# Kernel tuning notes

Measured on AMD Instinct MI355X. Metric: run time of the kernel, lower is better.

The kernel has to match this reference:

```python
import jax, jax.numpy as jnp
import numpy as np

B, N, E, DIN, DOUT = 8, 4096, 1024, 256, 256
EPS = 1e-8

def setup_inputs() -> dict:
    key = jax.random.key(0)
    k1, k2, k3, k4 = jax.random.split(key, 4)
    x = jax.random.normal(k1, (B, N, DIN), dtype=jnp.float32)
    H = jax.random.uniform(k2, (B, N, E), dtype=jnp.float32)
    weight = jax.random.normal(k3, (DIN, DOUT), dtype=jnp.float32) * (1.0 / np.sqrt(DOUT))
    bias = jax.random.normal(k4, (DOUT,), dtype=jnp.float32) * (1.0 / np.sqrt(DOUT))
    return {"x": x, "hypergraph_matrix": H, "weight": weight, "bias": bias}

def reference(x, hypergraph_matrix, weight, bias):
    H = hypergraph_matrix                      # [B, N, E]
    d_v = jnp.clip(jnp.sum(H, axis=2), EPS)    # node degrees [B, N]
    d_v_inv_sqrt = d_v ** -0.5
    d_e = jnp.clip(jnp.sum(H, axis=1), EPS)    # hyperedge degrees [B, E]
    d_e_inv = 1.0 / d_e
    # D_v^{-1/2} H D_e^{-1}
    step2 = d_v_inv_sqrt[:, :, None] * H * d_e_inv[:, None, :]   # [B, N, E]
    # (D_v^{-1/2} H D_e^{-1} H^T) D_v^{-1/2}  -- original materializes [B, N, N]
    step3 = jnp.einsum('bne,bme->bnm', step2, H)                 # [B, N, N]
    normalized_matrix = step3 * d_v_inv_sqrt[:, None, :]         # [B, N, N]
    support = jnp.einsum('bnd,df->bnf', x, weight)               # X Theta
    out = jnp.einsum('bnm,bmf->bnf', normalized_matrix, support) + bias
    # dropout is identity in eval / deterministic baseline
    return out
```

## Files before the change

kernel.cpp:

```cpp
#include <hip/hip_runtime.h>
#include <hip/hip_bf16.h>

#define BATCH 8
#define NN 4096
#define EE 1024
#define DIN 256
#define DOUT 256
#define EPS 1e-8f

typedef short bf16x8 __attribute__((ext_vector_type(8)));
typedef float f32x4 __attribute__((ext_vector_type(4)));

__device__ __forceinline__ unsigned short f2bf(float f) {
    unsigned u = __float_as_uint(f);
    return (unsigned short)((u + 0x7FFFu + ((u >> 16) & 1u)) >> 16);
}

__device__ __forceinline__ unsigned pk2(float lo, float hi) {
    __hip_bfloat162 h = __float22bfloat162_rn(float2{lo, hi});
    return *(unsigned*)&h;
}
__device__ __forceinline__ bf16x8 pack8(float4 a, float4 b) {
    union { bf16x8 v; unsigned u[4]; } r;
    r.u[0] = pk2(a.x, a.y); r.u[1] = pk2(a.z, a.w);
    r.u[2] = pk2(b.x, b.y); r.u[3] = pk2(b.z, b.w);
    return r.v;
}

__device__ __forceinline__ void g2l16(const void* g, void* l) {
    __builtin_amdgcn_global_load_lds(
        (const __attribute__((address_space(1))) unsigned*)g,
        (__attribute__((address_space(3))) unsigned*)l, 16, 0, 0);
}


template <int LD>
__device__ __forceinline__ void stage_tile(const unsigned short* src, int k0, short* lds, int tid) {
#pragma unroll
    for (int j = 0; j < 2; ++j) {
        int q = tid + j * 256;
        int r = q >> 2;
        int c = (q ^ (r >> 1)) & 3;
        g2l16(src + (size_t)r * LD + k0 + c * 8, (char*)lds + q * 16);
    }
}

__device__ __forceinline__ bf16x8 frag_ld(const short* lds, int r, int c) {
    int off = (r << 6) | (((c ^ (r >> 1)) & 3) << 4);
    return *(const bf16x8*)((const char*)lds + off);
}

template <int LDA, int LDB>
__device__ __forceinline__ void gemm_core(const unsigned short* A, const unsigned short* B,
                                          int kIters, int k0, f32x4 acc[4][4],
                                          short* As, short* Bs) {
    int tid = threadIdx.x, lane = tid & 63, wave = tid >> 6;
    int wm = (wave >> 1) * 64, wn = (wave & 1) * 64;
    int fr = lane & 15, fc = lane >> 4;
    for (int kt = 0; kt < kIters; ++kt) {
        int k = k0 + kt * 32;
        __syncthreads();
        stage_tile<LDA>(A, k, As, tid);
        stage_tile<LDB>(B, k, Bs, tid);
        __syncthreads();
        bf16x8 av[4], bv[4];
#pragma unroll
        for (int i = 0; i < 4; ++i) av[i] = frag_ld(As, wm + i * 16 + fr, fc);
#pragma unroll
        for (int j = 0; j < 4; ++j) bv[j] = frag_ld(Bs, wn + j * 16 + fr, fc);
#pragma unroll
        for (int i = 0; i < 4; ++i)
#pragma unroll
            for (int j = 0; j < 4; ++j)
                acc[i][j] = __builtin_amdgcn_mfma_f32_16x16x32_bf16(av[i], bv[j], acc[i][j], 0, 0, 0);
    }
}


__global__ __launch_bounds__(256) void prep_tr(const float* __restrict__ H,
                                               unsigned short* __restrict__ Ht,
                                               float* __restrict__ dv_acc,
                                               float* __restrict__ de_acc) {
    __shared__ float tile[64][65];
    int ns = blockIdx.x, et = blockIdx.y, b = blockIdx.z;
    int e0 = et * 64;
    int t = threadIdx.x;
    int r = t >> 2, cq = (t & 3) * 16;
    int c = t >> 2, q = (t & 3) * 16;
    float de_part = 0.f;
    for (int it = 0; it < 8; ++it) {
        int n0 = ns * 512 + it * 64;
        const float* src = H + ((size_t)(b * NN + n0 + r)) * EE + e0 + cq;
        float4 v0 = *(const float4*)(src + 0);
        float4 v1 = *(const float4*)(src + 4);
        float4 v2 = *(const float4*)(src + 8);
        float4 v3 = *(const float4*)(src + 12);
        float rs = v0.x + v0.y + v0.z + v0.w + v1.x + v1.y + v1.z + v1.w +
                   v2.x + v2.y + v2.z + v2.w + v3.x + v3.y + v3.z + v3.w;
        rs += __shfl_down(rs, 2);
        rs += __shfl_down(rs, 1);
        __syncthreads();
        tile[cq + 0][r] = v0.x;  tile[cq + 1][r] = v0.y;  tile[cq + 2][r] = v0.z;  tile[cq + 3][r] = v0.w;
        tile[cq + 4][r] = v1.x;  tile[cq + 5][r] = v1.y;  tile[cq + 6][r] = v1.z;  tile[cq + 7][r] = v1.w;
        tile[cq + 8][r] = v2.x;  tile[cq + 9][r] = v2.y;  tile[cq + 10][r] = v2.z; tile[cq + 11][r] = v2.w;
        tile[cq + 12][r] = v3.x; tile[cq + 13][r] = v3.y; tile[cq + 14][r] = v3.z; tile[cq + 15][r] = v3.w;
        if ((t & 3) == 0) atomicAdd(dv_acc + b * NN + n0 + r, rs);
        __syncthreads();
        float w[16];
#pragma unroll
        for (int j = 0; j < 16; ++j) { w[j] = tile[c][q + j]; de_part += w[j]; }
        bf16x8 p0 = pack8(float4{w[0], w[1], w[2], w[3]}, float4{w[4], w[5], w[6], w[7]});
        bf16x8 p1 = pack8(float4{w[8], w[9], w[10], w[11]}, float4{w[12], w[13], w[14], w[15]});
        unsigned short* dst = Ht + ((size_t)(b * EE + e0 + c)) * NN + n0 + q;
        *(bf16x8*)dst = p0; *(bf16x8*)(dst + 8) = p1;
    }
    de_part += __shfl_down(de_part, 2);
    de_part += __shfl_down(de_part, 1);
    if ((t & 3) == 0) atomicAdd(de_acc + b * EE + e0 + c, de_part);
}

__global__ __launch_bounds__(256) void prep_xw(const float* __restrict__ X,
                                               const float* __restrict__ W,
                                               unsigned short* __restrict__ Xb,
                                               unsigned short* __restrict__ Wt) {
    __shared__ float tile[64][65];
    int bid = blockIdx.x;
    int t = threadIdx.x;
    if (bid < 2048) {
        size_t base = ((size_t)bid * 256 + t) * 16;
        float4 a0 = *(const float4*)(X + base + 0);
        float4 a1 = *(const float4*)(X + base + 4);
        float4 a2 = *(const float4*)(X + base + 8);
        float4 a3 = *(const float4*)(X + base + 12);
        *(bf16x8*)(Xb + base) = pack8(a0, a1);
        *(bf16x8*)(Xb + base + 8) = pack8(a2, a3);
    } else {
        int w = bid - 2048;
        int k0 = (w >> 2) * 64, f0 = (w & 3) * 64;
        int r = t >> 2, cq = (t & 3) * 16;
#pragma unroll
        for (int j = 0; j < 16; j += 4) {
            float4 x4 = *(const float4*)(W + (size_t)(k0 + r) * DOUT + f0 + cq + j);
            tile[r][cq + j] = x4.x; tile[r][cq + j + 1] = x4.y;
            tile[r][cq + j + 2] = x4.z; tile[r][cq + j + 3] = x4.w;
        }
        __syncthreads();
        int c = t >> 2, rq = (t & 3) * 16;
        bf16x8 q0, q1;
#pragma unroll
        for (int j = 0; j < 16; ++j) {
            float x = tile[rq + j][c];
            if (j < 8) q0[j] = (short)f2bf(x); else q1[j - 8] = (short)f2bf(x);
        }
        unsigned short* dst = Wt + (size_t)(f0 + c) * DIN + k0 + rq;
        *(bf16x8*)dst = q0; *(bf16x8*)(dst + 8) = q1;
    }
}


__global__ __launch_bounds__(256) void mfma_xw(const unsigned short* __restrict__ Xb,
                                               const unsigned short* __restrict__ Wt,
                                               const float* __restrict__ dv_acc,
                                               unsigned short* __restrict__ Tt) {
    __shared__ short As[128 * 32], Bs[128 * 32];
    int m0 = blockIdx.x * 128, f0 = blockIdx.y * 128;
    f32x4 acc[4][4] = {};
    gemm_core<DIN, DIN>(Xb + (size_t)m0 * DIN, Wt + (size_t)f0 * DIN, DIN / 32, 0, acc, As, Bs);
    int lane = threadIdx.x & 63, wave = threadIdx.x >> 6;
    int wm = (wave >> 1) * 64, wn = (wave & 1) * 64;
    int rg = (lane >> 4) * 4, cl = lane & 15;
    int b = m0 >> 12, nb = m0 & (NN - 1);
#pragma unroll
    for (int i = 0; i < 4; ++i) {
        int rbase = wm + i * 16 + rg;
        float4 dv = *(const float4*)(dv_acc + m0 + rbase);
        float s0 = rsqrtf(fmaxf(dv.x, EPS)), s1 = rsqrtf(fmaxf(dv.y, EPS));
        float s2 = rsqrtf(fmaxf(dv.z, EPS)), s3 = rsqrtf(fmaxf(dv.w, EPS));
#pragma unroll
        for (int j = 0; j < 4; ++j) {
            int f = f0 + wn + j * 16 + cl;
            f32x4 a = acc[i][j];
            ushort4 o = { f2bf(a.x * s0), f2bf(a.y * s1), f2bf(a.z * s2), f2bf(a.w * s3) };
            *(ushort4*)(Tt + (((size_t)b * DOUT + f) << 12) + nb + rbase) = o;
        }
    }
}

__global__ __launch_bounds__(256) void mfma_ht(const unsigned short* __restrict__ Ht,
                                               const unsigned short* __restrict__ Tt,
                                               float* __restrict__ P) {
    __shared__ short As[128 * 32], Bs[128 * 32];
    int e0 = blockIdx.x * 128, f0 = blockIdx.y * 128;
    int b = blockIdx.z >> 2, s = blockIdx.z & 3;
    f32x4 acc[4][4] = {};
    gemm_core<NN, NN>(Ht + ((size_t)b * EE + e0) * NN, Tt + ((size_t)b * DOUT + f0) * NN,
                      1024 / 32, s * 1024, acc, As, Bs);
    int lane = threadIdx.x & 63, wave = threadIdx.x >> 6;
    int wm = (wave >> 1) * 64, wn = (wave & 1) * 64;
    int rg = (lane >> 4) * 4, cl = lane & 15;
    float* Pb = P + (size_t)s * (BATCH * DOUT * EE) + (size_t)b * (DOUT * EE);
#pragma unroll
    for (int i = 0; i < 4; ++i) {
        int e = e0 + wm + i * 16 + rg;
#pragma unroll
        for (int j = 0; j < 4; ++j) {
            int f = f0 + wn + j * 16 + cl;
            *(f32x4*)(Pb + (size_t)f * EE + e) = acc[i][j];
        }
    }
}

__global__ __launch_bounds__(256) void combine_u(const float* __restrict__ P,
                                                 const float* __restrict__ de_acc,
                                                 unsigned short* __restrict__ Ut) {
    const int PS = BATCH * DOUT * EE;
    int idx = (blockIdx.x * 256 + threadIdx.x) * 4;
    f32x4 s = *(const f32x4*)(P + idx);
    s += *(const f32x4*)(P + PS + idx);
    s += *(const f32x4*)(P + 2 * PS + idx);
    s += *(const f32x4*)(P + 3 * PS + idx);
    int b = idx >> 18, e = idx & (EE - 1);
    float4 de = *(const float4*)(de_acc + b * EE + e);
    ushort4 o = { f2bf(s.x / fmaxf(de.x, EPS)), f2bf(s.y / fmaxf(de.y, EPS)),
                  f2bf(s.z / fmaxf(de.z, EPS)), f2bf(s.w / fmaxf(de.w, EPS)) };
    *(ushort4*)(Ut + idx) = o;
}

__global__ __launch_bounds__(256) void mfma_hu(const unsigned short* __restrict__ Ut,
                                               const float* __restrict__ Hf,
                                               const float* __restrict__ dv_acc,
                                               const float* __restrict__ bias,
                                               float* __restrict__ out) {
    __shared__ short As[128 * 32], Bs[128 * 32];
    int f0 = blockIdx.x * 128, n0 = blockIdx.y * 128, b = blockIdx.z;
    const unsigned short* A = Ut + ((size_t)b * DOUT + f0) * EE;
    const float* Bsrc = Hf + ((size_t)(b * NN + n0)) * EE;
    int tid = threadIdx.x, lane = tid & 63, wave = tid >> 6;
    int wm = (wave >> 1) * 64, wn = (wave & 1) * 64;
    int fr = lane & 15, fc = lane >> 4;
    int br = tid >> 1, bh = tid & 1;
    f32x4 acc[4][4] = {};
    for (int kt = 0; kt < EE / 32; ++kt) {
        int k = kt * 32;
        __syncthreads();
        stage_tile<EE>(A, k, As, tid);
        const float* s = Bsrc + (size_t)br * EE + k + bh * 16;
        float4 x0 = *(const float4*)(s + 0);
        float4 x1 = *(const float4*)(s + 4);
        float4 x2 = *(const float4*)(s + 8);
        float4 x3 = *(const float4*)(s + 12);
        bf16x8 p0 = pack8(x0, x1), p1 = pack8(x2, x3);
        int c0 = 2 * bh, c1 = 2 * bh + 1;
        *(bf16x8*)((char*)Bs + (br << 6) + (((c0 ^ (br >> 1)) & 3) << 4)) = p0;
        *(bf16x8*)((char*)Bs + (br << 6) + (((c1 ^ (br >> 1)) & 3) << 4)) = p1;
        __syncthreads();
        bf16x8 av[4], bv[4];
#pragma unroll
        for (int i = 0; i < 4; ++i) av[i] = frag_ld(As, wm + i * 16 + fr, fc);
#pragma unroll
        for (int j = 0; j < 4; ++j) bv[j] = frag_ld(Bs, wn + j * 16 + fr, fc);
#pragma unroll
        for (int i = 0; i < 4; ++i)
#pragma unroll
            for (int j = 0; j < 4; ++j)
                acc[i][j] = __builtin_amdgcn_mfma_f32_16x16x32_bf16(av[i], bv[j], acc[i][j], 0, 0, 0);
    }
    int rg = (lane >> 4) * 4, cl = lane & 15;
    float dvv[4];
#pragma unroll
    for (int j = 0; j < 4; ++j) {
        int n = n0 + wn + j * 16 + cl;
        dvv[j] = rsqrtf(fmaxf(dv_acc[b * NN + n], EPS));
    }
#pragma unroll
    for (int i = 0; i < 4; ++i) {
        int f = f0 + wm + i * 16 + rg;
        float4 bi = *(const float4*)(bias + f);
#pragma unroll
        for (int j = 0; j < 4; ++j) {
            int n = n0 + wn + j * 16 + cl;
            f32x4 a = acc[i][j];
            float4 o = { a.x * dvv[j] + bi.x, a.y * dvv[j] + bi.y,
                         a.z * dvv[j] + bi.z, a.w * dvv[j] + bi.w };
            *(float4*)(out + (((size_t)b * NN + n) << 8) + f) = o;
        }
    }
}


__global__ __launch_bounds__(256) void dv_kernel(const float* __restrict__ H, float* __restrict__ dv_is) {
    int row = blockIdx.x * 4 + (threadIdx.x >> 6);
    int lane = threadIdx.x & 63;
    const float4* p = (const float4*)(H + (size_t)row * EE);
    float s = 0.f;
#pragma unroll
    for (int j = 0; j < 4; ++j) { float4 v = p[j * 64 + lane]; s += v.x + v.y + v.z + v.w; }
#pragma unroll
    for (int off = 32; off; off >>= 1) s += __shfl_down(s, off);
    if (lane == 0) dv_is[row] = rsqrtf(fmaxf(s, EPS));
}
__global__ void zero_kernel(float* __restrict__ p, int n) {
    int i = blockIdx.x * 256 + threadIdx.x;
    if (i < n) p[i] = 0.f;
}
__global__ __launch_bounds__(256) void de_kernel(const float* __restrict__ H, float* __restrict__ de_acc) {
    int b = blockIdx.x >> 4, chunk = blockIdx.x & 15;
    int e = blockIdx.y * 256 + threadIdx.x;
    const float* p = H + ((size_t)b * NN + chunk * 256) * EE + e;
    float s = 0.f;
    for (int n = 0; n < 256; ++n) s += p[(size_t)n * EE];
    atomicAdd(&de_acc[b * EE + e], s);
}
__global__ void de_finalize(float* __restrict__ de) {
    int i = blockIdx.x * 256 + threadIdx.x;
    de[i] = 1.0f / fmaxf(de[i], EPS);
}
__global__ __launch_bounds__(256) void gemm_xw(const float* __restrict__ X, const float* __restrict__ W,
                                               const float* __restrict__ dv_is, float* __restrict__ T) {
    int b = blockIdx.z;
    int m0 = blockIdx.x * 64, f0 = blockIdx.y * 64;
    const float* A = X + (size_t)b * NN * DIN;
    __shared__ float As[16][68];
    __shared__ float Bs[16][68];
    int tid = threadIdx.x;
    int ar = tid >> 2, ac = (tid & 3) << 2;
    int br = tid >> 4, bc = (tid & 15) << 2;
    int r0 = (tid >> 4) << 2, c0 = (tid & 15) << 2;
    float acc[4][4] = {};
    for (int k0 = 0; k0 < DIN; k0 += 16) {
        float4 av = *(const float4*)&A[(size_t)(m0 + ar) * DIN + k0 + ac];
        float4 bv = *(const float4*)&W[(size_t)(k0 + br) * DOUT + f0 + bc];
        __syncthreads();
        As[ac + 0][ar] = av.x; As[ac + 1][ar] = av.y; As[ac + 2][ar] = av.z; As[ac + 3][ar] = av.w;
        *(float4*)&Bs[br][bc] = bv;
        __syncthreads();
#pragma unroll
        for (int k = 0; k < 16; ++k) {
            float4 a4 = *(const float4*)&As[k][r0];
            float4 b4 = *(const float4*)&Bs[k][c0];
            float a[4] = {a4.x, a4.y, a4.z, a4.w};
            float bb[4] = {b4.x, b4.y, b4.z, b4.w};
#pragma unroll
            for (int i = 0; i < 4; ++i)
#pragma unroll
                for (int j = 0; j < 4; ++j) acc[i][j] = fmaf(a[i], bb[j], acc[i][j]);
        }
    }
#pragma unroll
    for (int i = 0; i < 4; ++i) {
        float dv = dv_is[b * NN + m0 + r0 + i];
        float4 o = {dv * acc[i][0], dv * acc[i][1], dv * acc[i][2], dv * acc[i][3]};
        *(float4*)&T[((size_t)b * NN + m0 + r0 + i) * DOUT + f0 + c0] = o;
    }
}
__global__ __launch_bounds__(256) void gemm_ht(const float* __restrict__ H, const float* __restrict__ T,
                                               const float* __restrict__ de_inv, float* __restrict__ U) {
    int b = blockIdx.z;
    int e0 = blockIdx.x * 64, f0 = blockIdx.y * 64;
    const float* Hb = H + (size_t)b * NN * EE;
    const float* Tb = T + (size_t)b * NN * DOUT;
    __shared__ float As[16][68];
    __shared__ float Bs[16][68];
    int tid = threadIdx.x;
    int lr = tid >> 4, lc = (tid & 15) << 2;
    int r0 = (tid >> 4) << 2, c0 = (tid & 15) << 2;
    float acc[4][4] = {};
    for (int n0 = 0; n0 < NN; n0 += 16) {
        float4 av = *(const float4*)&Hb[(size_t)(n0 + lr) * EE + e0 + lc];
        float4 bv = *(const float4*)&Tb[(size_t)(n0 + lr) * DOUT + f0 + lc];
        __syncthreads();
        *(float4*)&As[lr][lc] = av;
        *(float4*)&Bs[lr][lc] = bv;
        __syncthreads();
#pragma unroll
        for (int k = 0; k < 16; ++k) {
            float4 a4 = *(const float4*)&As[k][r0];
            float4 b4 = *(const float4*)&Bs[k][c0];
            float a[4] = {a4.x, a4.y, a4.z, a4.w};
            float bb[4] = {b4.x, b4.y, b4.z, b4.w};
#pragma unroll
            for (int i = 0; i < 4; ++i)
#pragma unroll
                for (int j = 0; j < 4; ++j) acc[i][j] = fmaf(a[i], bb[j], acc[i][j]);
        }
    }
#pragma unroll
    for (int i = 0; i < 4; ++i) {
        float de = de_inv[b * EE + e0 + r0 + i];
        float4 o = {de * acc[i][0], de * acc[i][1], de * acc[i][2], de * acc[i][3]};
        *(float4*)&U[((size_t)b * EE + e0 + r0 + i) * DOUT + f0 + c0] = o;
    }
}
__global__ __launch_bounds__(256) void gemm_hu(const float* __restrict__ H, const float* __restrict__ U,
                                               const float* __restrict__ dv_is, const float* __restrict__ bias,
                                               float* __restrict__ out) {
    int b = blockIdx.z;
    int n0 = blockIdx.x * 64, f0 = blockIdx.y * 64;
    const float* Hb = H + (size_t)b * NN * EE;
    const float* Ub = U + (size_t)b * EE * DOUT;
    __shared__ float As[16][68];
    __shared__ float Bs[16][68];
    int tid = threadIdx.x;
    int ar = tid >> 2, ac = (tid & 3) << 2;
    int br = tid >> 4, bc = (tid & 15) << 2;
    int r0 = (tid >> 4) << 2, c0 = (tid & 15) << 2;
    float acc[4][4] = {};
    for (int k0 = 0; k0 < EE; k0 += 16) {
        float4 av = *(const float4*)&Hb[(size_t)(n0 + ar) * EE + k0 + ac];
        float4 bv = *(const float4*)&Ub[(size_t)(k0 + br) * DOUT + f0 + bc];
        __syncthreads();
        As[ac + 0][ar] = av.x; As[ac + 1][ar] = av.y; As[ac + 2][ar] = av.z; As[ac + 3][ar] = av.w;
        *(float4*)&Bs[br][bc] = bv;
        __syncthreads();
#pragma unroll
        for (int k = 0; k < 16; ++k) {
            float4 a4 = *(const float4*)&As[k][r0];
            float4 b4 = *(const float4*)&Bs[k][c0];
            float a[4] = {a4.x, a4.y, a4.z, a4.w};
            float bb[4] = {b4.x, b4.y, b4.z, b4.w};
#pragma unroll
            for (int i = 0; i < 4; ++i)
#pragma unroll
                for (int j = 0; j < 4; ++j) acc[i][j] = fmaf(a[i], bb[j], acc[i][j]);
        }
    }
    float4 bi = *(const float4*)&bias[f0 + c0];
#pragma unroll
    for (int i = 0; i < 4; ++i) {
        float dv = dv_is[b * NN + n0 + r0 + i];
        float4 o = {dv * acc[i][0] + bi.x, dv * acc[i][1] + bi.y, dv * acc[i][2] + bi.z, dv * acc[i][3] + bi.w};
        *(float4*)&out[((size_t)b * NN + n0 + r0 + i) * DOUT + f0 + c0] = o;
    }
}

extern "C" void kernel_launch(void* const* d_in, const int* in_sizes, int n_in,
                              void* d_out, int out_size, void* d_ws, size_t ws_size,
                              hipStream_t stream) {
    const float* x    = (const float*)d_in[0];
    const float* H    = (const float*)d_in[1];
    const float* W    = (const float*)d_in[2];
    const float* bias = (const float*)d_in[3];
    float* out = (float*)d_out;

    const size_t NEED = (size_t)(BATCH * NN + BATCH * EE + 4 * BATCH * DOUT * EE) * 4 +
                        (size_t)(DIN * DOUT + BATCH * DOUT * EE + (size_t)BATCH * NN * EE) * 2;

    if (ws_size >= NEED) {
        float* dv_acc = (float*)d_ws;
        float* de_acc = dv_acc + BATCH * NN;
        float* P      = de_acc + BATCH * EE;
        unsigned short* Wt = (unsigned short*)(P + (size_t)4 * BATCH * DOUT * EE);
        unsigned short* Ut = Wt + DIN * DOUT;
        unsigned short* Ht = Ut + (size_t)BATCH * DOUT * EE;
        unsigned short* Xb = (unsigned short*)d_out;
        unsigned short* Tt = Xb + (size_t)BATCH * NN * DOUT;

        hipMemsetAsync(dv_acc, 0, (size_t)(BATCH * NN + BATCH * EE) * sizeof(float), stream);
        prep_tr<<<dim3(8, 16, 8), 256, 0, stream>>>(H, Ht, dv_acc, de_acc);
        prep_xw<<<2064, 256, 0, stream>>>(x, W, Xb, Wt);
        mfma_xw<<<dim3(256, 2), 256, 0, stream>>>(Xb, Wt, dv_acc, Tt);
        mfma_ht<<<dim3(8, 2, 32), 256, 0, stream>>>(Ht, Tt, P);
        combine_u<<<2048, 256, 0, stream>>>(P, de_acc, Ut);
        mfma_hu<<<dim3(2, 32, 8), 256, 0, stream>>>(Ut, H, dv_acc, bias, out);
    } else {
        float* ws = (float*)d_ws;
        float* dv_is = ws;
        float* de    = ws + BATCH * NN;
        float* U     = de + BATCH * EE;
        float* T = out;
        dv_kernel<<<BATCH * NN / 4, 256, 0, stream>>>(H, dv_is);
        zero_kernel<<<(BATCH * EE + 255) / 256, 256, 0, stream>>>(de, BATCH * EE);
        de_kernel<<<dim3(BATCH * 16, EE / 256), 256, 0, stream>>>(H, de);
        de_finalize<<<BATCH * EE / 256, 256, 0, stream>>>(de);
        gemm_xw<<<dim3(NN / 64, DOUT / 64, BATCH), 256, 0, stream>>>(x, W, dv_is, T);
        gemm_ht<<<dim3(EE / 64, DOUT / 64, BATCH), 256, 0, stream>>>(H, T, de, U);
        gemm_hu<<<dim3(NN / 64, DOUT / 64, BATCH), 256, 0, stream>>>(H, U, dv_is, bias, out);
    }
}
```

Baseline: 357.9 us.

## Emit bf16 H copy in prep, fuse X conversion into GEMM, halve split-K

```diff
diff --git a/kernel.cpp b/kernel.cpp
--- a/kernel.cpp
+++ b/kernel.cpp
@@ -77,7 +77,8 @@
 }
 
 
-__global__ __launch_bounds__(256) void prep_tr(const float* __restrict__ H,
+__global__ __launch_bounds__(256) void prep_h2(const float* __restrict__ H,
+                                               unsigned short* __restrict__ Hb,
                                                unsigned short* __restrict__ Ht,
                                                float* __restrict__ dv_acc,
                                                float* __restrict__ de_acc) {
@@ -88,13 +89,16 @@
     int r = t >> 2, cq = (t & 3) * 16;
     int c = t >> 2, q = (t & 3) * 16;
     float de_part = 0.f;
+    float4 v0, v1, v2, v3;
+    {
+        const float* src = H + ((size_t)(b * NN + ns * 512 + r)) * EE + e0 + cq;
+        v0 = *(const float4*)(src + 0);
+        v1 = *(const float4*)(src + 4);
+        v2 = *(const float4*)(src + 8);
+        v3 = *(const float4*)(src + 12);
+    }
     for (int it = 0; it < 8; ++it) {
         int n0 = ns * 512 + it * 64;
-        const float* src = H + ((size_t)(b * NN + n0 + r)) * EE + e0 + cq;
-        float4 v0 = *(const float4*)(src + 0);
-        float4 v1 = *(const float4*)(src + 4);
-        float4 v2 = *(const float4*)(src + 8);
-        float4 v3 = *(const float4*)(src + 12);
         float rs = v0.x + v0.y + v0.z + v0.w + v1.x + v1.y + v1.z + v1.w +
                    v2.x + v2.y + v2.z + v2.w + v3.x + v3.y + v3.z + v3.w;
         rs += __shfl_down(rs, 2);
@@ -104,8 +108,18 @@
         tile[cq + 4][r] = v1.x;  tile[cq + 5][r] = v1.y;  tile[cq + 6][r] = v1.z;  tile[cq + 7][r] = v1.w;
         tile[cq + 8][r] = v2.x;  tile[cq + 9][r] = v2.y;  tile[cq + 10][r] = v2.z; tile[cq + 11][r] = v2.w;
         tile[cq + 12][r] = v3.x; tile[cq + 13][r] = v3.y; tile[cq + 14][r] = v3.z; tile[cq + 15][r] = v3.w;
+        unsigned short* hd = Hb + ((size_t)(b * NN + n0 + r)) * EE + e0 + cq;
+        *(bf16x8*)hd = pack8(v0, v1);
+        *(bf16x8*)(hd + 8) = pack8(v2, v3);
         if ((t & 3) == 0) atomicAdd(dv_acc + b * NN + n0 + r, rs);
         __syncthreads();
+        if (it < 7) {
+            const float* src = H + ((size_t)(b * NN + n0 + 64 + r)) * EE + e0 + cq;
+            v0 = *(const float4*)(src + 0);
+            v1 = *(const float4*)(src + 4);
+            v2 = *(const float4*)(src + 8);
+            v3 = *(const float4*)(src + 12);
+        }
         float w[16];
 #pragma unroll
         for (int j = 0; j < 16; ++j) { w[j] = tile[c][q + j]; de_part += w[j]; }
@@ -119,55 +133,70 @@
     if ((t & 3) == 0) atomicAdd(de_acc + b * EE + e0 + c, de_part);
 }
 
-__global__ __launch_bounds__(256) void prep_xw(const float* __restrict__ X,
-                                               const float* __restrict__ W,
-                                               unsigned short* __restrict__ Xb,
-                                               unsigned short* __restrict__ Wt) {
+__global__ __launch_bounds__(256) void prep_w(const float* __restrict__ W,
+                                              unsigned short* __restrict__ Wt) {
     __shared__ float tile[64][65];
-    int bid = blockIdx.x;
+    int w = blockIdx.x;
+    int k0 = (w >> 2) * 64, f0 = (w & 3) * 64;
     int t = threadIdx.x;
-    if (bid < 2048) {
-        size_t base = ((size_t)bid * 256 + t) * 16;
-        float4 a0 = *(const float4*)(X + base + 0);
-        float4 a1 = *(const float4*)(X + base + 4);
-        float4 a2 = *(const float4*)(X + base + 8);
-        float4 a3 = *(const float4*)(X + base + 12);
-        *(bf16x8*)(Xb + base) = pack8(a0, a1);
-        *(bf16x8*)(Xb + base + 8) = pack8(a2, a3);
-    } else {
-        int w = bid - 2048;
-        int k0 = (w >> 2) * 64, f0 = (w & 3) * 64;
-        int r = t >> 2, cq = (t & 3) * 16;
-#pragma unroll
-        for (int j = 0; j < 16; j += 4) {
-            float4 x4 = *(const float4*)(W + (size_t)(k0 + r) * DOUT + f0 + cq + j);
-            tile[r][cq + j] = x4.x; tile[r][cq + j + 1] = x4.y;
-            tile[r][cq + j + 2] = x4.z; tile[r][cq + j + 3] = x4.w;
-        }
-        __syncthreads();
-        int c = t >> 2, rq = (t & 3) * 16;
-        bf16x8 q0, q1;
-#pragma unroll
-        for (int j = 0; j < 16; ++j) {
-            float x = tile[rq + j][c];
-            if (j < 8) q0[j] = (short)f2bf(x); else q1[j - 8] = (short)f2bf(x);
-        }
-        unsigned short* dst = Wt + (size_t)(f0 + c) * DIN + k0 + rq;
-        *(bf16x8*)dst = q0; *(bf16x8*)(dst + 8) = q1;
-    }
-}
-
-
-__global__ __launch_bounds__(256) void mfma_xw(const unsigned short* __restrict__ Xb,
+    int r = t >> 2, cq = (t & 3) * 16;
+#pragma unroll
+    for (int j = 0; j < 16; j += 4) {
+        float4 x4 = *(const float4*)(W + (size_t)(k0 + r) * DOUT + f0 + cq + j);
+        tile[r][cq + j] = x4.x; tile[r][cq + j + 1] = x4.y;
+        tile[r][cq + j + 2] = x4.z; tile[r][cq + j + 3] = x4.w;
+    }
+    __syncthreads();
+    int c = t >> 2, rq = (t & 3) * 16;
+    bf16x8 q0, q1;
+#pragma unroll
+    for (int j = 0; j < 16; ++j) {
+        float x = tile[rq + j][c];
+        if (j < 8) q0[j] = (short)f2bf(x); else q1[j - 8] = (short)f2bf(x);
+    }
+    unsigned short* dst = Wt + (size_t)(f0 + c) * DIN + k0 + rq;
+    *(bf16x8*)dst = q0; *(bf16x8*)(dst + 8) = q1;
+}
+
+
+__global__ __launch_bounds__(256) void mfma_xw(const float* __restrict__ X,
                                                const unsigned short* __restrict__ Wt,
                                                const float* __restrict__ dv_acc,
                                                unsigned short* __restrict__ Tt) {
     __shared__ short As[128 * 32], Bs[128 * 32];
     int m0 = blockIdx.x * 128, f0 = blockIdx.y * 128;
+    const float* Asrc = X + (size_t)m0 * DIN;
+    const unsigned short* Bsrc = Wt + (size_t)f0 * DIN;
+    int tid = threadIdx.x, lane = tid & 63, wave = tid >> 6;
+    int wm = (wave >> 1) * 64, wn = (wave & 1) * 64;
+    int fr = lane & 15, fc = lane >> 4;
+    int ar = tid >> 1, ah = tid & 1;
     f32x4 acc[4][4] = {};
-    gemm_core<DIN, DIN>(Xb + (size_t)m0 * DIN, Wt + (size_t)f0 * DIN, DIN / 32, 0, acc, As, Bs);
-    int lane = threadIdx.x & 63, wave = threadIdx.x >> 6;
-    int wm = (wave >> 1) * 64, wn = (wave & 1) * 64;
+    for (int kt = 0; kt < DIN / 32; ++kt) {
+        int k = kt * 32;
+        __syncthreads();
+        stage_tile<DIN>(Bsrc, k, Bs, tid);
+        const float* s = Asrc + (size_t)ar * DIN + k + ah * 16;
+        float4 x0 = *(const float4*)(s + 0);
+        float4 x1 = *(const float4*)(s + 4);
+        float4 x2 = *(const float4*)(s + 8);
+        float4 x3 = *(const float4*)(s + 12);
+        bf16x8 p0 = pack8(x0, x1), p1 = pack8(x2, x3);
+        int c0 = 2 * ah, c1 = 2 * ah + 1;
+        *(bf16x8*)((char*)As + (ar << 6) + (((c0 ^ (ar >> 1)) & 3) << 4)) = p0;
+        *(bf16x8*)((char*)As + (ar << 6) + (((c1 ^ (ar >> 1)) & 3) << 4)) = p1;
+        __syncthreads();
+        bf16x8 av[4], bv[4];
+#pragma unroll
+        for (int i = 0; i < 4; ++i) av[i] = frag_ld(As, wm + i * 16 + fr, fc);
+#pragma unroll
+        for (int j = 0; j < 4; ++j) bv[j] = frag_ld(Bs, wn + j * 16 + fr, fc);
+#pragma unroll
+        for (int i = 0; i < 4; ++i)
+#pragma unroll
+            for (int j = 0; j < 4; ++j)
+                acc[i][j] = __builtin_amdgcn_mfma_f32_16x16x32_bf16(av[i], bv[j], acc[i][j], 0, 0, 0);
+    }
     int rg = (lane >> 4) * 4, cl = lane & 15;
     int b = m0 >> 12, nb = m0 & (NN - 1);
 #pragma unroll
@@ -191,10 +220,10 @@
                                                float* __restrict__ P) {
     __shared__ short As[128 * 32], Bs[128 * 32];
     int e0 = blockIdx.x * 128, f0 = blockIdx.y * 128;
-    int b = blockIdx.z >> 2, s = blockIdx.z & 3;
+    int b = blockIdx.z >> 1, s = blockIdx.z & 1;
     f32x4 acc[4][4] = {};
     gemm_core<NN, NN>(Ht + ((size_t)b * EE + e0) * NN, Tt + ((size_t)b * DOUT + f0) * NN,
-                      1024 / 32, s * 1024, acc, As, Bs);
+                      2048 / 32, s * 2048, acc, As, Bs);
     int lane = threadIdx.x & 63, wave = threadIdx.x >> 6;
     int wm = (wave >> 1) * 64, wn = (wave & 1) * 64;
     int rg = (lane >> 4) * 4, cl = lane & 15;
@@ -217,8 +246,6 @@
     int idx = (blockIdx.x * 256 + threadIdx.x) * 4;
     f32x4 s = *(const f32x4*)(P + idx);
     s += *(const f32x4*)(P + PS + idx);
-    s += *(const f32x4*)(P + 2 * PS + idx);
-    s += *(const f32x4*)(P + 3 * PS + idx);
     int b = idx >> 18, e = idx & (EE - 1);
     float4 de = *(const float4*)(de_acc + b * EE + e);
     ushort4 o = { f2bf(s.x / fmaxf(de.x, EPS)), f2bf(s.y / fmaxf(de.y, EPS)),
@@ -227,44 +254,17 @@
 }
 
 __global__ __launch_bounds__(256) void mfma_hu(const unsigned short* __restrict__ Ut,
-                                               const float* __restrict__ Hf,
+                                               const unsigned short* __restrict__ Hb,
                                                const float* __restrict__ dv_acc,
                                                const float* __restrict__ bias,
                                                float* __restrict__ out) {
     __shared__ short As[128 * 32], Bs[128 * 32];
     int f0 = blockIdx.x * 128, n0 = blockIdx.y * 128, b = blockIdx.z;
-    const unsigned short* A = Ut + ((size_t)b * DOUT + f0) * EE;
-    const float* Bsrc = Hf + ((size_t)(b * NN + n0)) * EE;
-    int tid = threadIdx.x, lane = tid & 63, wave = tid >> 6;
+    f32x4 acc[4][4] = {};
+    gemm_core<EE, EE>(Ut + ((size_t)b * DOUT + f0) * EE, Hb + ((size_t)b * NN + n0) * EE,
+                      EE / 32, 0, acc, As, Bs);
+    int lane = threadIdx.x & 63, wave = threadIdx.x >> 6;
     int wm = (wave >> 1) * 64, wn = (wave & 1) * 64;
-    int fr = lane & 15, fc = lane >> 4;
-    int br = tid >> 1, bh = tid & 1;
-    f32x4 acc[4][4] = {};
-    for (int kt = 0; kt < EE / 32; ++kt) {
-        int k = kt * 32;
-        __syncthreads();
-        stage_tile<EE>(A, k, As, tid);
-        const float* s = Bsrc + (size_t)br * EE + k + bh * 16;
-        float4 x0 = *(const float4*)(s + 0);
-        float4 x1 = *(const float4*)(s + 4);
-        float4 x2 = *(const float4*)(s + 8);
-        float4 x3 = *(const float4*)(s + 12);
-        bf16x8 p0 = pack8(x0, x1), p1 = pack8(x2, x3);
-        int c0 = 2 * bh, c1 = 2 * bh + 1;
-        *(bf16x8*)((char*)Bs + (br << 6) + (((c0 ^ (br >> 1)) & 3) << 4)) = p0;
-        *(bf16x8*)((char*)Bs + (br << 6) + (((c1 ^ (br >> 1)) & 3) << 4)) = p1;
-        __syncthreads();
-        bf16x8 av[4], bv[4];
-#pragma unroll
-        for (int i = 0; i < 4; ++i) av[i] = frag_ld(As, wm + i * 16 + fr, fc);
-#pragma unroll
-        for (int j = 0; j < 4; ++j) bv[j] = frag_ld(Bs, wn + j * 16 + fr, fc);
-#pragma unroll
-        for (int i = 0; i < 4; ++i)
-#pragma unroll
-            for (int j = 0; j < 4; ++j)
-                acc[i][j] = __builtin_amdgcn_mfma_f32_16x16x32_bf16(av[i], bv[j], acc[i][j], 0, 0, 0);
-    }
     int rg = (lane >> 4) * 4, cl = lane & 15;
     float dvv[4];
 #pragma unroll
@@ -442,26 +442,27 @@
     const float* bias = (const float*)d_in[3];
     float* out = (float*)d_out;
 
-    const size_t NEED = (size_t)(BATCH * NN + BATCH * EE + 4 * BATCH * DOUT * EE) * 4 +
-                        (size_t)(DIN * DOUT + BATCH * DOUT * EE + (size_t)BATCH * NN * EE) * 2;
+    const size_t NEED = (size_t)(BATCH * NN + BATCH * EE + 2 * BATCH * DOUT * EE) * 4 +
+                        ((size_t)DIN * DOUT + (size_t)BATCH * DOUT * EE +
+                         2 * (size_t)BATCH * NN * EE + (size_t)BATCH * DOUT * NN) * 2;
 
     if (ws_size >= NEED) {
         float* dv_acc = (float*)d_ws;
         float* de_acc = dv_acc + BATCH * NN;
         float* P      = de_acc + BATCH * EE;
-        unsigned short* Wt = (unsigned short*)(P + (size_t)4 * BATCH * DOUT * EE);
+        unsigned short* Wt = (unsigned short*)(P + (size_t)2 * BATCH * DOUT * EE);
         unsigned short* Ut = Wt + DIN * DOUT;
-        unsigned short* Ht = Ut + (size_t)BATCH * DOUT * EE;
-        unsigned short* Xb = (unsigned short*)d_out;
-        unsigned short* Tt = Xb + (size_t)BATCH * NN * DOUT;
+        unsigned short* Hb = Ut + (size_t)BATCH * DOUT * EE;
+        unsigned short* Ht = Hb + (size_t)BATCH * NN * EE;
+        unsigned short* Tt = Ht + (size_t)BATCH * NN * EE;
 
         hipMemsetAsync(dv_acc, 0, (size_t)(BATCH * NN + BATCH * EE) * sizeof(float), stream);
-        prep_tr<<<dim3(8, 16, 8), 256, 0, stream>>>(H, Ht, dv_acc, de_acc);
-        prep_xw<<<2064, 256, 0, stream>>>(x, W, Xb, Wt);
-        mfma_xw<<<dim3(256, 2), 256, 0, stream>>>(Xb, Wt, dv_acc, Tt);
-        mfma_ht<<<dim3(8, 2, 32), 256, 0, stream>>>(Ht, Tt, P);
+        prep_h2<<<dim3(8, 16, 8), 256, 0, stream>>>(H, Hb, Ht, dv_acc, de_acc);
+        prep_w<<<16, 256, 0, stream>>>(W, Wt);
+        mfma_xw<<<dim3(256, 2), 256, 0, stream>>>(x, Wt, dv_acc, Tt);
+        mfma_ht<<<dim3(8, 2, 16), 256, 0, stream>>>(Ht, Tt, P);
         combine_u<<<2048, 256, 0, stream>>>(P, de_acc, Ut);
-        mfma_hu<<<dim3(2, 32, 8), 256, 0, stream>>>(Ut, H, dv_acc, bias, out);
+        mfma_hu<<<dim3(2, 32, 8), 256, 0, stream>>>(Ut, Hb, dv_acc, bias, out);
     } else {
         float* ws = (float*)d_ws;
         float* dv_is = ws;
```

Result: slower. 368.9 us (+3.1%).
